# Kernel optimization log

Measured on AMD Instinct MI355X. Metric: run time of the kernel, lower is better.

## Reference

```python
import jax, jax.numpy as jnp
import numpy as np

N, D, M_COLS, K = 4096, 512, 4096, 2048

def setup_inputs() -> dict:
    key = jax.random.key(0)
    k1, k2, k3 = jax.random.split(key, 3)
    return {
        "in_activations": jax.random.normal(k1, (N, D), dtype=jnp.float32),
        "M": jax.random.normal(k2, (D, M_COLS), dtype=jnp.float32),
        "centroids": jax.random.normal(k3, (K, D), dtype=jnp.float32),
    }

def reference(in_activations, M, centroids):
    # dist[k, m] = || X @ (M[:, m] - c_k) ||_2  over the n sampled activations.
    # Expand || a - b ||^2 = ||a||^2 - 2 a.b + ||b||^2 with a = X@M[:,m], b = X@c_k
    # to avoid materializing the [K, n, m] broadcast tensor of the original.
    XM = in_activations @ M                 # [n, m]
    XC = in_activations @ centroids.T      # [n, K]
    sq = (jnp.sum(XM * XM, axis=0)[None, :]          # [1, m]
          - 2.0 * (XC.T @ XM)                        # [K, m]
          + jnp.sum(XC * XC, axis=0)[:, None])       # [K, 1]
    return jnp.sqrt(jnp.maximum(sq, 0.0))            # [K, m]
```

## Files before the change

### kernel.cpp

```cpp
#include <hip/hip_runtime.h>
#include <stdint.h>

#define NR    4096
#define D_DIM 512
#define MC    4096
#define KC    2048

typedef unsigned short u16;
typedef __attribute__((ext_vector_type(8))) short bf16x8;
typedef __attribute__((ext_vector_type(4))) float f32x4;

__device__ __forceinline__ u16 f2bf(float f) {
  union { float f; uint32_t u; } v; v.f = f;
  return (u16)((v.u + 0x7FFFu + ((v.u >> 16) & 1u)) >> 16);
}
__device__ __forceinline__ float bf2f(u16 h) {
  union { uint32_t u; float f; } v; v.u = (uint32_t)h << 16; return v.f;
}
__device__ __forceinline__ void gload16(const void* g, void* lds) {
  __builtin_amdgcn_global_load_lds((const __attribute__((address_space(1))) void*)g,
                                   (__attribute__((address_space(3))) void*)lds,
                                   16, 0, 0);
}

template <int EPI>
__device__ __forceinline__ void gemm_tile(
    const u16* __restrict__ Ag, const u16* __restrict__ Bg,
    float* __restrict__ Cf, u16* __restrict__ Cbf,
    const u16* __restrict__ DotH, const float* __restrict__ DotF,
    float* __restrict__ vatom, const float* __restrict__ tv, const float* __restrict__ sv,
    int m0, int n0, int Ndim, int Kdim, int kBeg, int kEnd,
    u16* As0, u16* As1, u16* Bs0, u16* Bs1, int tid)
{
  const int rowt = tid >> 3;
  const int cswz = ((tid & 7) ^ ((tid >> 3) & 7)) << 3;
  const int wave = tid >> 6, lane = tid & 63;
  const int wr = (wave >> 1) << 6, wc = (wave & 1) << 6;
  const int fr = lane & 15;
  const int sw = fr & 7;
  const int hq = lane >> 4;
  const int wb = wave << 10;

  f32x4 acc[4][4] = {};
  const u16* agB = Ag + (size_t)(m0 + rowt) * Kdim + cswz;
  const u16* bgB = Bg + (size_t)(n0 + rowt) * Kdim + cswz;

  #define STAGE(k0, Asb, Bsb)                                          \
    _Pragma("unroll")                                                  \
    for (int c = 0; c < 4; ++c) {                                      \
      gload16(agB + (k0) + (size_t)(c * 32) * Kdim, (char*)(Asb) + c * 4096 + wb); \
      gload16(bgB + (k0) + (size_t)(c * 32) * Kdim, (char*)(Bsb) + c * 4096 + wb); \
    }

  STAGE(kBeg, As0, Bs0)
  __syncthreads();

  const int nt = (kEnd - kBeg) >> 6;
  for (int t = 0; t < nt; ++t) {
    u16* Ac = (t & 1) ? As1 : As0;
    u16* Bc = (t & 1) ? Bs1 : Bs0;
    if (t + 1 < nt) {
      u16* An = (t & 1) ? As0 : As1;
      u16* Bn = (t & 1) ? Bs0 : Bs1;
      STAGE(kBeg + (t + 1) * 64, An, Bn)
    }
    #pragma unroll
    for (int kk = 0; kk < 64; kk += 32) {
      const int so = ((((kk >> 3) + hq) ^ sw) << 3);
      bf16x8 a[4], b[4];
      #pragma unroll
      for (int i = 0; i < 4; ++i) a[i] = *(const bf16x8*)&Ac[(wr + i * 16 + fr) * 64 + so];
      #pragma unroll
      for (int j = 0; j < 4; ++j) b[j] = *(const bf16x8*)&Bc[(wc + j * 16 + fr) * 64 + so];
      #pragma unroll
      for (int i = 0; i < 4; ++i)
        #pragma unroll
        for (int j = 0; j < 4; ++j)
          acc[i][j] = __builtin_amdgcn_mfma_f32_16x16x32_bf16(a[i], b[j], acc[i][j], 0, 0, 0);
    }
    __syncthreads();
  }
  #undef STAGE

  const int q = lane >> 4;
  #pragma unroll
  for (int i = 0; i < 4; ++i) {
    #pragma unroll
    for (int r = 0; r < 4; ++r) {
      const int grow = m0 + wr + i * 16 + q * 4 + r;
      float p = 0.f;
      #pragma unroll
      for (int j = 0; j < 4; ++j) {
        const int gcol = n0 + wc + j * 16 + fr;
        const float v = acc[i][j][r];
        const size_t idx = (size_t)grow * Ndim + gcol;
        if (EPI == 0) Cf[idx] = v;
        if (EPI == 2) { float sq = tv[gcol] - 2.f * v + sv[grow]; Cf[idx] = sqrtf(fmaxf(sq, 0.f)); }
        if (EPI == 3) { Cbf[idx] = f2bf(v); p += v * bf2f(DotH[idx]); }
        if (EPI == 4) { p += v * DotF[idx]; }
      }
      if (EPI == 3 || EPI == 4) {
        #pragma unroll
        for (int off = 1; off < 16; off <<= 1) p += __shfl_xor(p, off);
        if (fr == 0) atomicAdd(&vatom[grow], p);
      }
    }
  }
}

__device__ __forceinline__ void transpose_tile(
    const float* __restrict__ in, u16* __restrict__ out, int R, int C,
    int rt, int ct, int tid, float* tile )
{
  const int tx = tid & 31, ty = tid >> 5;
  #pragma unroll
  for (int i = 0; i < 32; i += 8)
    tile[(size_t)(ty + i) * 33 + tx] = in[(size_t)(rt + ty + i) * C + ct + tx];
  __syncthreads();
  #pragma unroll
  for (int i = 0; i < 32; i += 8)
    out[(size_t)(ct + ty + i) * R + rt + tx] = f2bf(tile[(size_t)tx * 33 + ty + i]);
  __syncthreads();
}

__global__ __launch_bounds__(256)
void prep(const float* __restrict__ X, const float* __restrict__ Mm,
          const float* __restrict__ Cc,
          u16* __restrict__ XT_bf, u16* __restrict__ M_bfT, u16* __restrict__ C_bf,
          float* __restrict__ tvec)
{
  __shared__ float tile[32 * 33];
  const int b = blockIdx.x, tid = threadIdx.x;
  if (b < 512) {
    #pragma unroll 1
    for (int j = 0; j < 4; ++j) {
      int T = b * 4 + j;
      transpose_tile(X, XT_bf, NR, D_DIM, (T >> 4) * 32, (T & 15) * 32, tid, tile);
    }
  } else if (b < 1024) {
    #pragma unroll 1
    for (int j = 0; j < 4; ++j) {
      int T = (b - 512) * 4 + j;
      transpose_tile(Mm, M_bfT, D_DIM, MC, (T >> 7) * 32, (T & 127) * 32, tid, tile);
    }
  } else {
    const int bb = b - 1024;
    int zi = bb * 256 + tid;
    if (zi < 4096 + 2048) tvec[zi] = 0.f;
    const float4* C4 = (const float4*)Cc;
    #pragma unroll 1
    for (int i = bb * 256 + tid; i < (KC * D_DIM) / 4; i += 128 * 256) {
      float4 v = C4[i];
      ushort4 r; r.x = f2bf(v.x); r.y = f2bf(v.y); r.z = f2bf(v.z); r.w = f2bf(v.w);
      *(ushort4*)&C_bf[(size_t)i * 4] = r;
    }
  }
}

__global__ __launch_bounds__(256)
void g_gemm(const u16* __restrict__ XT_bf, float* __restrict__ Gpart)
{
  __shared__ __align__(16) u16 As[2][8192];
  __shared__ __align__(16) u16 Bs[2][8192];
  const int t = blockIdx.x, z = blockIdx.y;
  const int n0 = (t & 3) * 128, m0 = (t >> 2) * 128;
  gemm_tile<0>(XT_bf, XT_bf, Gpart + (size_t)z * 512 * 512, nullptr, nullptr, nullptr,
               nullptr, nullptr, nullptr, m0, n0, 512, NR, z * 256, z * 256 + 256,
               As[0], As[1], Bs[0], Bs[1], threadIdx.x);
}

__global__ __launch_bounds__(256)
void reduce_g(const float* __restrict__ Gpart, u16* __restrict__ G_bf)
{
  const float4* P4 = (const float4*)Gpart;
  int i = blockIdx.x * 256 + threadIdx.x;
  float4 s = {0.f, 0.f, 0.f, 0.f};
  #pragma unroll
  for (int z = 0; z < 16; ++z) {
    float4 v = P4[(size_t)z * (512 * 512 / 4) + i];
    s.x += v.x; s.y += v.y; s.z += v.z; s.w += v.w;
  }
  ushort4 r; r.x = f2bf(s.x); r.y = f2bf(s.y); r.z = f2bf(s.z); r.w = f2bf(s.w);
  *(ushort4*)&G_bf[(size_t)i * 4] = r;
}

__global__ __launch_bounds__(256)
void mid(const u16* __restrict__ M_bfT, const u16* __restrict__ C_bf,
         const u16* __restrict__ G_bf, const float* __restrict__ Cc,
         u16* __restrict__ A_bfT, float* __restrict__ tvec)
{
  __shared__ __align__(16) u16 As[2][8192];
  __shared__ __align__(16) u16 Bs[2][8192];
  const int b = blockIdx.x, tid = threadIdx.x;
  if (b < 128) {
    const int n0 = (b & 3) * 128, m0 = (b >> 2) * 128;
    gemm_tile<3>(M_bfT, G_bf, nullptr, A_bfT, M_bfT, nullptr, tvec, nullptr, nullptr,
                 m0, n0, 512, 512, 0, 512, As[0], As[1], Bs[0], Bs[1], tid);
  } else {
    const int u = b - 128;
    const int n0 = (u & 3) * 128, m0 = (u >> 2) * 128;
    gemm_tile<4>(C_bf, G_bf, nullptr, nullptr, nullptr, Cc, tvec + 4096, nullptr, nullptr,
                 m0, n0, 512, 512, 0, 512, As[0], As[1], Bs[0], Bs[1], tid);
  }
}

__global__ __launch_bounds__(256)
void final_gemm(const u16* __restrict__ C_bf, const u16* __restrict__ A_bfT,
                const float* __restrict__ tvec, float* __restrict__ out)
{
  __shared__ __align__(16) u16 As[2][8192];
  __shared__ __align__(16) u16 Bs[2][8192];
  const int n0 = blockIdx.x * 128, m0 = blockIdx.y * 128;
  gemm_tile<2>(C_bf, A_bfT, out, nullptr, nullptr, nullptr, nullptr, tvec, tvec + 4096,
               m0, n0, MC, 512, 0, 512, As[0], As[1], Bs[0], Bs[1], threadIdx.x);
}

extern "C" void kernel_launch(void* const* d_in, const int* in_sizes, int n_in,
                              void* d_out, int out_size, void* d_ws, size_t ws_size,
                              hipStream_t stream) {
  const float* X  = (const float*)d_in[0];
  const float* Mm = (const float*)d_in[1];
  const float* Cc = (const float*)d_in[2];
  float* out = (float*)d_out;

  char* ws = (char*)d_ws;
  const size_t MB = 1u << 20;
  u16*   XT_bf = (u16*)(ws);
  u16*   C_bf  = (u16*)(ws + 4 * MB);
  u16*   M_bfT = (u16*)(ws + 6 * MB);
  u16*   A_bfT = (u16*)(ws + 10 * MB);
  u16*   G_bf  = (u16*)(ws + 14 * MB);
  float* tvec  = (float*)(ws + 14 * MB + 512 * 1024);
  float* Gpart = (float*)(ws + 15 * MB);

  prep<<<1152, 256, 0, stream>>>(X, Mm, Cc, XT_bf, M_bfT, C_bf, tvec);
  g_gemm<<<dim3(16, 16), 256, 0, stream>>>(XT_bf, Gpart);
  reduce_g<<<256, 256, 0, stream>>>(Gpart, G_bf);
  mid<<<192, 256, 0, stream>>>(M_bfT, C_bf, G_bf, Cc, A_bfT, tvec);
  final_gemm<<<dim3(32, 16), 256, 0, stream>>>(C_bf, A_bfT, tvec, out);
}
```

Baseline: 130.6 us.

## Overlap M/C conversion with split-K Gram GEMM and fix GEMM step counts

Splits the prep kernel so only the X transpose (plus zeroing tvec) runs first. The M transpose and centroid bf16 conversion now run inside the same launch as the split-K X^T X Gram GEMM, reusing the GEMM's LDS for the transpose tile, so that memory-bound conversion overlaps with MFMA work. The GEMM K-loop trip count becomes a template constant and is fully unrolled. This adds register pressure and code size, and the mixed-role blocks can leave the launch imbalanced.

```diff
diff --git a/kernel.cpp b/kernel.cpp
--- a/kernel.cpp
+++ b/kernel.cpp
@@ -23,13 +23,13 @@
                                    16, 0, 0);
 }
 
-template <int EPI>
+template <int EPI, int STEPS>
 __device__ __forceinline__ void gemm_tile(
     const u16* __restrict__ Ag, const u16* __restrict__ Bg,
     float* __restrict__ Cf, u16* __restrict__ Cbf,
     const u16* __restrict__ DotH, const float* __restrict__ DotF,
     float* __restrict__ vatom, const float* __restrict__ tv, const float* __restrict__ sv,
-    int m0, int n0, int Ndim, int Kdim, int kBeg, int kEnd,
+    int m0, int n0, int Ndim, int Kdim, int kBeg,
     u16* As0, u16* As1, u16* Bs0, u16* Bs1, int tid)
 {
   const int rowt = tid >> 3;
@@ -55,11 +55,11 @@
   STAGE(kBeg, As0, Bs0)
   __syncthreads();
 
-  const int nt = (kEnd - kBeg) >> 6;
-  for (int t = 0; t < nt; ++t) {
+  #pragma unroll
+  for (int t = 0; t < STEPS; ++t) {
     u16* Ac = (t & 1) ? As1 : As0;
     u16* Bc = (t & 1) ? Bs1 : Bs0;
-    if (t + 1 < nt) {
+    if (t + 1 < STEPS) {
       u16* An = (t & 1) ? As0 : As1;
       u16* Bn = (t & 1) ? Bs0 : Bs1;
       STAGE(kBeg + (t + 1) * 64, An, Bn)
@@ -124,29 +124,43 @@
 }
 
 __global__ __launch_bounds__(256)
-void prep(const float* __restrict__ X, const float* __restrict__ Mm,
-          const float* __restrict__ Cc,
-          u16* __restrict__ XT_bf, u16* __restrict__ M_bfT, u16* __restrict__ C_bf,
-          float* __restrict__ tvec)
+void xprep(const float* __restrict__ X, u16* __restrict__ XT_bf,
+           float* __restrict__ tvec)
 {
   __shared__ float tile[32 * 33];
   const int b = blockIdx.x, tid = threadIdx.x;
-  if (b < 512) {
+  int zi = b * 256 + tid;
+  if (zi < 4096 + 2048) tvec[zi] = 0.f;
+  #pragma unroll 1
+  for (int j = 0; j < 4; ++j) {
+    int T = b * 4 + j;
+    transpose_tile(X, XT_bf, NR, D_DIM, (T >> 4) * 32, (T & 15) * 32, tid, tile);
+  }
+}
+
+__global__ __launch_bounds__(256)
+void gmc(const u16* __restrict__ XT_bf, float* __restrict__ Gpart,
+         const float* __restrict__ Mm, const float* __restrict__ Cc,
+         u16* __restrict__ M_bfT, u16* __restrict__ C_bf)
+{
+  __shared__ __align__(16) u16 As[2][8192];
+  __shared__ __align__(16) u16 Bs[2][8192];
+  const int b = blockIdx.x, tid = threadIdx.x;
+  if (b < 256) {
+    const int t = b & 15, z = b >> 4;
+    const int n0 = (t & 3) * 128, m0 = (t >> 2) * 128;
+    gemm_tile<0, 4>(XT_bf, XT_bf, Gpart + (size_t)z * 512 * 512, nullptr, nullptr,
+                    nullptr, nullptr, nullptr, nullptr, m0, n0, 512, NR, z * 256,
+                    As[0], As[1], Bs[0], Bs[1], tid);
+  } else if (b < 768) {
+    float* ttile = (float*)As;
     #pragma unroll 1
     for (int j = 0; j < 4; ++j) {
-      int T = b * 4 + j;
-      transpose_tile(X, XT_bf, NR, D_DIM, (T >> 4) * 32, (T & 15) * 32, tid, tile);
-    }
-  } else if (b < 1024) {
-    #pragma unroll 1
-    for (int j = 0; j < 4; ++j) {
-      int T = (b - 512) * 4 + j;
-      transpose_tile(Mm, M_bfT, D_DIM, MC, (T >> 7) * 32, (T & 127) * 32, tid, tile);
+      int T = (b - 256) * 4 + j;
+      transpose_tile(Mm, M_bfT, D_DIM, MC, (T >> 7) * 32, (T & 127) * 32, tid, ttile);
     }
   } else {
-    const int bb = b - 1024;
-    int zi = bb * 256 + tid;
-    if (zi < 4096 + 2048) tvec[zi] = 0.f;
+    const int bb = b - 768;
     const float4* C4 = (const float4*)Cc;
     #pragma unroll 1
     for (int i = bb * 256 + tid; i < (KC * D_DIM) / 4; i += 128 * 256) {
@@ -158,18 +172,6 @@
 }
 
 __global__ __launch_bounds__(256)
-void g_gemm(const u16* __restrict__ XT_bf, float* __restrict__ Gpart)
-{
-  __shared__ __align__(16) u16 As[2][8192];
-  __shared__ __align__(16) u16 Bs[2][8192];
-  const int t = blockIdx.x, z = blockIdx.y;
-  const int n0 = (t & 3) * 128, m0 = (t >> 2) * 128;
-  gemm_tile<0>(XT_bf, XT_bf, Gpart + (size_t)z * 512 * 512, nullptr, nullptr, nullptr,
-               nullptr, nullptr, nullptr, m0, n0, 512, NR, z * 256, z * 256 + 256,
-               As[0], As[1], Bs[0], Bs[1], threadIdx.x);
-}
-
-__global__ __launch_bounds__(256)
 void reduce_g(const float* __restrict__ Gpart, u16* __restrict__ G_bf)
 {
   const float4* P4 = (const float4*)Gpart;
@@ -194,13 +196,13 @@
   const int b = blockIdx.x, tid = threadIdx.x;
   if (b < 128) {
     const int n0 = (b & 3) * 128, m0 = (b >> 2) * 128;
-    gemm_tile<3>(M_bfT, G_bf, nullptr, A_bfT, M_bfT, nullptr, tvec, nullptr, nullptr,
-                 m0, n0, 512, 512, 0, 512, As[0], As[1], Bs[0], Bs[1], tid);
+    gemm_tile<3, 8>(M_bfT, G_bf, nullptr, A_bfT, M_bfT, nullptr, tvec, nullptr, nullptr,
+                    m0, n0, 512, 512, 0, As[0], As[1], Bs[0], Bs[1], tid);
   } else {
     const int u = b - 128;
     const int n0 = (u & 3) * 128, m0 = (u >> 2) * 128;
-    gemm_tile<4>(C_bf, G_bf, nullptr, nullptr, nullptr, Cc, tvec + 4096, nullptr, nullptr,
-                 m0, n0, 512, 512, 0, 512, As[0], As[1], Bs[0], Bs[1], tid);
+    gemm_tile<4, 8>(C_bf, G_bf, nullptr, nullptr, nullptr, Cc, tvec + 4096, nullptr,
+                    nullptr, m0, n0, 512, 512, 0, As[0], As[1], Bs[0], Bs[1], tid);
   }
 }
 
@@ -211,8 +213,9 @@
   __shared__ __align__(16) u16 As[2][8192];
   __shared__ __align__(16) u16 Bs[2][8192];
   const int n0 = blockIdx.x * 128, m0 = blockIdx.y * 128;
-  gemm_tile<2>(C_bf, A_bfT, out, nullptr, nullptr, nullptr, nullptr, tvec, tvec + 4096,
-               m0, n0, MC, 512, 0, 512, As[0], As[1], Bs[0], Bs[1], threadIdx.x);
+  gemm_tile<2, 8>(C_bf, A_bfT, out, nullptr, nullptr, nullptr, nullptr, tvec,
+                  tvec + 4096, m0, n0, MC, 512, 0,
+                  As[0], As[1], Bs[0], Bs[1], threadIdx.x);
 }
 
 extern "C" void kernel_launch(void* const* d_in, const int* in_sizes, int n_in,
@@ -233,8 +236,8 @@
   float* tvec  = (float*)(ws + 14 * MB + 512 * 1024);
   float* Gpart = (float*)(ws + 15 * MB);
 
-  prep<<<1152, 256, 0, stream>>>(X, Mm, Cc, XT_bf, M_bfT, C_bf, tvec);
-  g_gemm<<<dim3(16, 16), 256, 0, stream>>>(XT_bf, Gpart);
+  xprep<<<512, 256, 0, stream>>>(X, XT_bf, tvec);
+  gmc<<<896, 256, 0, stream>>>(XT_bf, Gpart, Mm, Cc, M_bfT, C_bf);
   reduce_g<<<256, 256, 0, stream>>>(Gpart, G_bf);
   mid<<<192, 256, 0, stream>>>(M_bfT, C_bf, G_bf, Cc, A_bfT, tvec);
   final_gemm<<<dim3(32, 16), 256, 0, stream>>>(C_bf, A_bfT, tvec, out);
```

Result: no change. 132.0 us (+1.0%).
